# Kernel optimization log

Hardware: AMD Instinct MI355X
Metric: run time of the kernel (lower is better)

Reference implementation:

```python
import jax, jax.numpy as jnp
import numpy as np


def setup_inputs() -> dict:
    key = jax.random.key(0)
    B, L, H, D = 4, 4096, 8, 64
    sample_k = int(np.ceil(np.log(L)))  # factor=1 -> U_part = ceil(ln L_K) = 9
    k1, k2, k3, k4 = jax.random.split(key, 4)
    return {
        "queries": jax.random.normal(k1, (B, L, H, D), jnp.float32),
        "keys": jax.random.normal(k2, (B, L, H, D), jnp.float32),
        "values": jax.random.normal(k3, (B, L, H, D), jnp.float32),
        "index_sample": jax.random.randint(k4, (L, sample_k), 0, L),
    }


def _prob_attention(Q, K, V, index_sample):
    # Q, K, V: [B, H, L, D]
    B, H, L_K, D = K.shape
    L_Q = Q.shape[2]
    u = min(int(np.ceil(np.log(L_Q))), L_Q)  # n_top (static)

    # --- _prob_QK: sampled scores, sparsity measure M, top-u queries ---
    # gather sampled keys per query position: [B, H, L_Q, sample_k, D]
    K_sample = K[:, :, index_sample, :]
    QK_sample = jnp.einsum('bhld,bhlsd->bhls', Q, K_sample)  # [B,H,L_Q,S]
    M = QK_sample.max(axis=-1) - QK_sample.sum(axis=-1) / L_K  # [B,H,L_Q]
    _, M_top = jax.lax.top_k(M, u)  # [B,H,u] indices of top queries

    Q_reduce = jnp.take_along_axis(Q, M_top[..., None], axis=2)  # [B,H,u,D]
    scale = 1.0 / jnp.sqrt(jnp.asarray(D, Q.dtype))
    scores = jnp.einsum('bhud,bhkd->bhuk', Q_reduce, K) * scale  # [B,H,u,L_K]

    # --- initial context (mask_flag=False): mean of V over keys ---
    context = jnp.broadcast_to(V.mean(axis=2, keepdims=True), (B, H, L_Q, D))

    # --- update context at the top-u query positions ---
    attn = jax.nn.softmax(scores, axis=-1)  # [B,H,u,L_K]
    ctx_top = jnp.einsum('bhuk,bhkd->bhud', attn, V)  # [B,H,u,D]
    b_idx = jnp.arange(B)[:, None, None]
    h_idx = jnp.arange(H)[None, :, None]
    context = context.at[b_idx, h_idx, M_top].set(ctx_top)
    return context, attn


def reference(queries, keys, values, index_sample):
    # inputs: [B, L, H, D] -> internal [B, H, L, D]
    Q = queries.transpose(0, 2, 1, 3)
    K = keys.transpose(0, 2, 1, 3)
    V = values.transpose(0, 2, 1, 3)
    context, attn = _prob_attention(Q, K, V, index_sample)
    return context.transpose(0, 2, 1, 3), attn
```

## Files before the change

kernel.cpp:

```cpp
#include <hip/hip_runtime.h>
#include <math.h>

#define B_ 4
#define L_ 4096
#define H_ 8
#define D_ 64
#define S_ 9
#define U_ 9
#define VC_ 64
#define CC_ 16
#define TKC_ 8
#define KCH_ 32
#define SCB_ (B_ * (L_ / KCH_))

#define VMBLK_ 256
#define MBLK_ 4096
#define FILLBLK_ 8192

__device__ __forceinline__ float dot4(const float4& a, const float4& b) {
    return a.x * b.x + a.y * b.y + a.z * b.z + a.w * b.w;
}

__global__ void __launch_bounds__(256, 4)
kernel_M_vmean(const float* __restrict__ Q, const float* __restrict__ K,
               const int* __restrict__ idx, float* __restrict__ M,
               const float* __restrict__ V, float* __restrict__ vpart) {
    if (blockIdx.x < VMBLK_) {
        int blk = blockIdx.x;
        int c = blk & (VC_ - 1), b = blk >> 6;
        int col = threadIdx.x & 127;
        int lp  = threadIdx.x >> 7;
        const int CHUNK = L_ / VC_;
        const float4* base = (const float4*)(V + (size_t)b * L_ * H_ * D_);
        float4 acc = make_float4(0.f, 0.f, 0.f, 0.f);
        for (int l = c * CHUNK + lp; l < (c + 1) * CHUNK; l += 2) {
            float4 v = base[(size_t)l * 128 + col];
            acc.x += v.x; acc.y += v.y; acc.z += v.z; acc.w += v.w;
        }
        __shared__ float4 red[256];
        red[threadIdx.x] = acc;
        __syncthreads();
        if (lp == 0) {
            float4 o = red[threadIdx.x + 128];
            acc.x += o.x; acc.y += o.y; acc.z += o.z; acc.w += o.w;
            ((float4*)vpart)[(size_t)blk * 128 + col] = acc;
        }
        return;
    }
    int t = threadIdx.x;
    int wid = t >> 6, lane = t & 63;
    int w = ((blockIdx.x - VMBLK_) << 2) + wid;
    int b = __builtin_amdgcn_readfirstlane(w >> 12);
    int l = __builtin_amdgcn_readfirstlane(w & (L_ - 1));

    int ki[S_];
#pragma unroll
    for (int s = 0; s < S_; ++s) ki[s] = idx[l * S_ + s];

    const float4* qb = (const float4*)(Q + (size_t)(b * L_ + l) * (H_ * D_));
    float4 q0 = qb[2 * lane];
    float4 q1 = qb[2 * lane + 1];

    const float* Kb = K + (size_t)b * L_ * (H_ * D_);

    float4 ka[S_], kc[S_];
#pragma unroll
    for (int s = 0; s < S_; ++s) {
        const float4* kp = (const float4*)(Kb + (size_t)ki[s] * (H_ * D_));
        ka[s] = kp[2 * lane];
        kc[s] = kp[2 * lane + 1];
    }

    float mx = -INFINITY, sm = 0.0f;
#pragma unroll
    for (int s = 0; s < S_; ++s) {
        float d = dot4(q0, ka[s]) + dot4(q1, kc[s]);
        d += __shfl_xor(d, 1);
        d += __shfl_xor(d, 2);
        d += __shfl_xor(d, 4);
        mx = fmaxf(mx, d);
        sm += d;
    }
    if ((lane & 7) == 0) {
        int h = lane >> 3;
        M[((size_t)(b * H_ + h) << 12) + l] = mx - sm * (1.0f / (float)L_);
    }
}

#define CSWAP(a, b)                                                          \
    if (v[b] > v[a] || (v[b] == v[a] && id[b] < id[a])) {                    \
        float tv = v[a]; v[a] = v[b]; v[b] = tv;                             \
        int ti = id[a]; id[a] = id[b]; id[b] = ti;                           \
    }

__global__ void kernel_topk1(const float* __restrict__ M,
                             float* __restrict__ cand_v, int* __restrict__ cand_i) {
    int bh = blockIdx.x >> 3;
    int chunk = blockIdx.x & (TKC_ - 1);
    int lane = threadIdx.x;
    const float* Ms = M + ((size_t)bh << 12);

    float v[8]; int id[8];
#pragma unroll
    for (int c = 0; c < 8; ++c) {
        int gi = chunk * 512 + lane + 64 * c;
        v[c] = Ms[gi]; id[c] = gi;
    }
    CSWAP(0,1) CSWAP(2,3) CSWAP(4,5) CSWAP(6,7)
    CSWAP(0,2) CSWAP(1,3) CSWAP(4,6) CSWAP(5,7)
    CSWAP(1,2) CSWAP(5,6)
    CSWAP(0,4) CSWAP(1,5) CSWAP(2,6) CSWAP(3,7)
    CSWAP(2,4) CSWAP(3,5)
    CSWAP(1,2) CSWAP(3,4) CSWAP(5,6)

    float* cv = cand_v + (size_t)blockIdx.x * U_;
    int*   ci = cand_i + (size_t)blockIdx.x * U_;
#pragma unroll
    for (int r = 0; r < U_; ++r) {
        float bv = v[0]; int bi = id[0];
#pragma unroll
        for (int off = 1; off < 64; off <<= 1) {
            float ov = __shfl_xor(bv, off);
            int   oi = __shfl_xor(bi, off);
            if (ov > bv || (ov == bv && oi < bi)) { bv = ov; bi = oi; }
        }
        if (lane == 0) { cv[r] = bv; ci[r] = bi; }
        if (id[0] == bi) {
#pragma unroll
            for (int c = 0; c < 7; ++c) { v[c] = v[c+1]; id[c] = id[c+1]; }
            v[7] = -INFINITY; id[7] = 0x7fffffff;
        }
    }
}

__global__ void kernel_small(const float* __restrict__ cand_v, const int* __restrict__ cand_i,
                             int* __restrict__ Mtop, const float* __restrict__ vpart,
                             float* __restrict__ vmean) {
    if (blockIdx.x >= 32) {
        int bh = blockIdx.x - 32;
        int h = bh & (H_ - 1), b = bh >> 3;
        int d = threadIdx.x;
        float s = 0.0f;
        for (int c = 0; c < VC_; ++c)
            s += vpart[(size_t)(b * VC_ + c) * (H_ * D_) + h * D_ + d];
        vmean[bh * D_ + d] = s * (1.0f / (float)L_);
        return;
    }
    int bh = blockIdx.x;
    int lane = threadIdx.x;
    const float* cv = cand_v + (size_t)bh * (TKC_ * U_);
    const int*   ci = cand_i + (size_t)bh * (TKC_ * U_);

    float v[2]; int id[2];
    v[0] = cv[lane]; id[0] = ci[lane];
    if (lane < TKC_ * U_ - 64) { v[1] = cv[64 + lane]; id[1] = ci[64 + lane]; }
    else { v[1] = -INFINITY; id[1] = 0x7fffffff; }
    CSWAP(0,1)

#pragma unroll
    for (int r = 0; r < U_; ++r) {
        float bv = v[0]; int bi = id[0];
#pragma unroll
        for (int off = 1; off < 64; off <<= 1) {
            float ov = __shfl_xor(bv, off);
            int   oi = __shfl_xor(bi, off);
            if (ov > bv || (ov == bv && oi < bi)) { bv = ov; bi = oi; }
        }
        if (lane == 0) Mtop[bh * U_ + r] = bi;
        if (id[0] == bi) { v[0] = v[1]; id[0] = id[1]; v[1] = -INFINITY; id[1] = 0x7fffffff; }
    }
}

__global__ void __launch_bounds__(256, 4)
kernel_fill_scores(float* __restrict__ out, const float* __restrict__ vmean,
                   const float* __restrict__ Q, const float* __restrict__ K,
                   const int* __restrict__ Mtop, float* __restrict__ raw) {
    if (blockIdx.x < FILLBLK_) {
        int i = blockIdx.x * 256 + threadIdx.x;
        int d4 = i & 15;
        int h  = (i >> 4) & (H_ - 1);
        int b  = i >> (4 + 3 + 12);
        ((float4*)out)[i] = ((const float4*)vmean)[(b * H_ + h) * 16 + d4];
        return;
    }
    int n = blockIdx.x - FILLBLK_;
    int b = n >> 7;
    int chunk = n & 127;
    int k0 = chunk * KCH_;

    int t = threadIdx.x;
    int w = t >> 6, lane = t & 63;
    int h = lane >> 3, dq = lane & 7;
    int bh = b * H_ + h;

    float4 q0[U_], q1[U_];
#pragma unroll
    for (int u = 0; u < U_; ++u) {
        int mi = Mtop[bh * U_ + u];
        const float4* qp = (const float4*)(Q + (size_t)((b * L_ + mi) * H_ + h) * D_);
        q0[u] = qp[2 * dq];
        q1[u] = qp[2 * dq + 1];
    }

    __shared__ float sc[H_][U_][KCH_ + 1];

    const float* Kb = K + (size_t)b * L_ * (H_ * D_);
    const float4* kp = (const float4*)(Kb + (size_t)(k0 + w * 8) * (H_ * D_));
    float4 kv0 = kp[2 * lane], kv1 = kp[2 * lane + 1];
#pragma unroll
    for (int i = 0; i < 8; ++i) {
        int kloc = w * 8 + i;
        float4 nv0, nv1;
        if (i < 7) {
            const float4* np = (const float4*)(Kb + (size_t)(k0 + kloc + 1) * (H_ * D_));
            nv0 = np[2 * lane]; nv1 = np[2 * lane + 1];
        }
        float p[U_];
#pragma unroll
        for (int u = 0; u < U_; ++u) {
            float d = dot4(q0[u], kv0) + dot4(q1[u], kv1);
            d += __shfl_xor(d, 1);
            d += __shfl_xor(d, 2);
            d += __shfl_xor(d, 4);
            p[u] = d;
        }
        float val = p[0];
#pragma unroll
        for (int u = 1; u < 8; ++u) val = (dq == u) ? p[u] : val;
        sc[h][dq][kloc] = val;
        if (dq == 0) sc[h][8][kloc] = p[8];
        kv0 = nv0; kv1 = nv1;
    }
    __syncthreads();

#pragma unroll
    for (int r = 0; r < 9; ++r) {
        int j = r * 256 + t;
        int kloc = j & 31;
        int hu = j >> 5;
        int h2 = hu / U_, u2 = hu - h2 * U_;
        raw[((size_t)(b * H_ + h2) * U_ + u2) * L_ + k0 + kloc] =
            sc[h2][u2][kloc] * 0.125f;
    }
}

__global__ void kernel_softmax(float* __restrict__ attn) {
    int row = blockIdx.x;
    float4* a = (float4*)(attn + (size_t)row * L_);
    int t = threadIdx.x;

    float4 v[4];
    float mx = -INFINITY;
#pragma unroll
    for (int i = 0; i < 4; ++i) {
        v[i] = a[t + 256 * i];
        mx = fmaxf(mx, fmaxf(fmaxf(v[i].x, v[i].y), fmaxf(v[i].z, v[i].w)));
    }
    __shared__ float red[256];
    __shared__ float bmax, bsum;
    red[t] = mx;
    __syncthreads();
    for (int off = 128; off > 0; off >>= 1) {
        if (t < off) red[t] = fmaxf(red[t], red[t + off]);
        __syncthreads();
    }
    if (t == 0) bmax = red[0];
    __syncthreads();

    float mm = bmax, sum = 0.0f;
#pragma unroll
    for (int i = 0; i < 4; ++i) {
        v[i].x = expf(v[i].x - mm); v[i].y = expf(v[i].y - mm);
        v[i].z = expf(v[i].z - mm); v[i].w = expf(v[i].w - mm);
        sum += v[i].x + v[i].y + v[i].z + v[i].w;
    }
    red[t] = sum;
    __syncthreads();
    for (int off = 128; off > 0; off >>= 1) {
        if (t < off) red[t] += red[t + off];
        __syncthreads();
    }
    if (t == 0) bsum = red[0];
    __syncthreads();

    float inv = 1.0f / bsum;
#pragma unroll
    for (int i = 0; i < 4; ++i) {
        v[i].x *= inv; v[i].y *= inv; v[i].z *= inv; v[i].w *= inv;
        a[t + 256 * i] = v[i];
    }
}

__global__ void kernel_ctxf(const float* __restrict__ attn, const float* __restrict__ V,
                            float* __restrict__ cpart) {
    int n = blockIdx.x;
    int x = n & 7, m = n >> 3;
    int chunk = m & (CC_ - 1);
    int bh = (m >> 4) * 8 + x;
    int h = bh & (H_ - 1), b = bh >> 3;
    int k0 = chunk * (L_ / CC_);

    int t = threadIdx.x;
    int g = t >> 6, lane = t & 63;
    int kl = lane >> 4, d4 = lane & 15;
    const float* abase = attn + (size_t)bh * U_ * L_;

    float4 acc[U_];
#pragma unroll
    for (int u = 0; u < U_; ++u) acc[u] = make_float4(0.f, 0.f, 0.f, 0.f);

    for (int i = 0; i < 16; ++i) {
        int k = k0 + (g * 4 + kl) + 16 * i;
        float4 vv = *(const float4*)(V + (size_t)((b * L_ + k) * H_ + h) * D_ + 4 * d4);
        float av[U_];
#pragma unroll
        for (int u = 0; u < U_; ++u) av[u] = abase[(size_t)u * L_ + k];
#pragma unroll
        for (int u = 0; u < U_; ++u) {
            acc[u].x += av[u] * vv.x; acc[u].y += av[u] * vv.y;
            acc[u].z += av[u] * vv.z; acc[u].w += av[u] * vv.w;
        }
    }
#pragma unroll
    for (int u = 0; u < U_; ++u) {
        acc[u].x += __shfl_xor(acc[u].x, 16); acc[u].y += __shfl_xor(acc[u].y, 16);
        acc[u].z += __shfl_xor(acc[u].z, 16); acc[u].w += __shfl_xor(acc[u].w, 16);
        acc[u].x += __shfl_xor(acc[u].x, 32); acc[u].y += __shfl_xor(acc[u].y, 32);
        acc[u].z += __shfl_xor(acc[u].z, 32); acc[u].w += __shfl_xor(acc[u].w, 32);
    }
    __shared__ float4 red[U_][4][16];
    if (kl == 0) {
#pragma unroll
        for (int u = 0; u < U_; ++u) red[u][g][d4] = acc[u];
    }
    __syncthreads();
    if (t < U_ * 16) {
        int u = t >> 4, dd = t & 15;
        float4 s0 = red[u][0][dd], s1 = red[u][1][dd];
        float4 s2 = red[u][2][dd], s3 = red[u][3][dd];
        float4 s = make_float4(s0.x + s1.x + s2.x + s3.x, s0.y + s1.y + s2.y + s3.y,
                               s0.z + s1.z + s2.z + s3.z, s0.w + s1.w + s2.w + s3.w);
        ((float4*)cpart)[((size_t)(bh * CC_ + chunk) * U_ + u) * 16 + dd] = s;
    }
}

__global__ void kernel_ctx2(const float* __restrict__ cpart, const int* __restrict__ Mtop,
                            float* __restrict__ out) {
    int row = blockIdx.x;
    int u = row % U_, bh = row / U_;
    int h = bh & (H_ - 1), b = bh >> 3;
    int d = threadIdx.x;
    float s = 0.0f;
#pragma unroll
    for (int c = 0; c < CC_; ++c)
        s += cpart[((size_t)(bh * CC_ + c) * U_ + u) * 64 + d];
    int l = Mtop[bh * U_ + u];
    out[(size_t)((b * L_ + l) * H_ + h) * D_ + d] = s;
}

extern "C" void kernel_launch(void* const* d_in, const int* in_sizes, int n_in,
                              void* d_out, int out_size, void* d_ws, size_t ws_size,
                              hipStream_t stream) {
    const float* Q   = (const float*)d_in[0];
    const float* K   = (const float*)d_in[1];
    const float* V   = (const float*)d_in[2];
    const int*   idx = (const int*)d_in[3];

    float* ctx_out  = (float*)d_out;
    float* attn_out = (float*)d_out + (size_t)B_ * L_ * H_ * D_;

    float* M      = (float*)d_ws;
    float* vpart  = M + (size_t)B_ * H_ * L_;
    float* vmean  = vpart + (size_t)B_ * VC_ * H_ * D_;
    float* cpart  = vmean + B_ * H_ * D_;
    float* cand_v = cpart + (size_t)32 * CC_ * U_ * 64;
    int*   cand_i = (int*)(cand_v + 32 * TKC_ * U_);
    int*   Mtop   = cand_i + 32 * TKC_ * U_;

    kernel_M_vmean<<<VMBLK_ + MBLK_, 256, 0, stream>>>(Q, K, idx, M, V, vpart);
    kernel_topk1<<<B_ * H_ * TKC_, 64, 0, stream>>>(M, cand_v, cand_i);
    kernel_small<<<64, 64, 0, stream>>>(cand_v, cand_i, Mtop, vpart, vmean);
    kernel_fill_scores<<<FILLBLK_ + SCB_, 256, 0, stream>>>(ctx_out, vmean, Q, K, Mtop, attn_out);
    kernel_softmax<<<B_ * H_ * U_, 256, 0, stream>>>(attn_out);
    kernel_ctxf<<<32 * CC_, 256, 0, stream>>>(attn_out, V, cpart);
    kernel_ctx2<<<B_ * H_ * U_, 64, 0, stream>>>(cpart, Mtop, ctx_out);
}
```

Before: 195.7 us.

## Fuse softmax into score and context kernels using per-chunk online max/sum stats

Removes the standalone softmax kernel. The score kernel now writes per-chunk (max, sum-exp) statistics for each 32-key chunk. The context kernel merges these into global softmax stats, normalizes its slice of attention in place, and stages it in shared memory for the V product. This drops one launch and one full read/write pass over attention, at the cost of redundant stat merging in every ctx block and extra expf work.

```diff
diff --git a/kernel.cpp b/kernel.cpp
--- a/kernel.cpp
+++ b/kernel.cpp
@@ -11,7 +11,8 @@
 #define CC_ 16
 #define TKC_ 8
 #define KCH_ 32
-#define SCB_ (B_ * (L_ / KCH_))
+#define NCHK_ (L_ / KCH_)
+#define SCB_ (B_ * NCHK_)
 
 #define VMBLK_ 256
 #define MBLK_ 4096
@@ -174,7 +175,8 @@
 __global__ void __launch_bounds__(256, 4)
 kernel_fill_scores(float* __restrict__ out, const float* __restrict__ vmean,
                    const float* __restrict__ Q, const float* __restrict__ K,
-                   const int* __restrict__ Mtop, float* __restrict__ raw) {
+                   const int* __restrict__ Mtop, float* __restrict__ raw,
+                   float* __restrict__ stats) {
     if (blockIdx.x < FILLBLK_) {
         int i = blockIdx.x * 256 + threadIdx.x;
         int d4 = i & 15;
@@ -242,57 +244,23 @@
         raw[((size_t)(b * H_ + h2) * U_ + u2) * L_ + k0 + kloc] =
             sc[h2][u2][kloc] * 0.125f;
     }
-}
-
-__global__ void kernel_softmax(float* __restrict__ attn) {
-    int row = blockIdx.x;
-    float4* a = (float4*)(attn + (size_t)row * L_);
-    int t = threadIdx.x;
-
-    float4 v[4];
-    float mx = -INFINITY;
-#pragma unroll
-    for (int i = 0; i < 4; ++i) {
-        v[i] = a[t + 256 * i];
-        mx = fmaxf(mx, fmaxf(fmaxf(v[i].x, v[i].y), fmaxf(v[i].z, v[i].w)));
-    }
-    __shared__ float red[256];
-    __shared__ float bmax, bsum;
-    red[t] = mx;
-    __syncthreads();
-    for (int off = 128; off > 0; off >>= 1) {
-        if (t < off) red[t] = fmaxf(red[t], red[t + off]);
-        __syncthreads();
-    }
-    if (t == 0) bmax = red[0];
-    __syncthreads();
-
-    float mm = bmax, sum = 0.0f;
-#pragma unroll
-    for (int i = 0; i < 4; ++i) {
-        v[i].x = expf(v[i].x - mm); v[i].y = expf(v[i].y - mm);
-        v[i].z = expf(v[i].z - mm); v[i].w = expf(v[i].w - mm);
-        sum += v[i].x + v[i].y + v[i].z + v[i].w;
-    }
-    red[t] = sum;
-    __syncthreads();
-    for (int off = 128; off > 0; off >>= 1) {
-        if (t < off) red[t] += red[t + off];
-        __syncthreads();
-    }
-    if (t == 0) bsum = red[0];
-    __syncthreads();
-
-    float inv = 1.0f / bsum;
-#pragma unroll
-    for (int i = 0; i < 4; ++i) {
-        v[i].x *= inv; v[i].y *= inv; v[i].z *= inv; v[i].w *= inv;
-        a[t + 256 * i] = v[i];
-    }
-}
-
-__global__ void kernel_ctxf(const float* __restrict__ attn, const float* __restrict__ V,
-                            float* __restrict__ cpart) {
+
+    if (t < H_ * U_) {
+        int h2 = t / U_, u2 = t - h2 * U_;
+        float mxs = -INFINITY;
+#pragma unroll
+        for (int k = 0; k < KCH_; ++k) mxs = fmaxf(mxs, sc[h2][u2][k]);
+        mxs *= 0.125f;
+        float se = 0.0f;
+#pragma unroll
+        for (int k = 0; k < KCH_; ++k) se += expf(sc[h2][u2][k] * 0.125f - mxs);
+        ((float2*)stats)[(size_t)((b * H_ + h2) * U_ + u2) * NCHK_ + chunk] =
+            make_float2(mxs, se);
+    }
+}
+
+__global__ void kernel_ctxf(float* __restrict__ attn, const float* __restrict__ stats,
+                            const float* __restrict__ V, float* __restrict__ cpart) {
     int n = blockIdx.x;
     int x = n & 7, m = n >> 3;
     int chunk = m & (CC_ - 1);
@@ -301,20 +269,57 @@
     int k0 = chunk * (L_ / CC_);
 
     int t = threadIdx.x;
+
+    __shared__ float2 gstat[U_];
+    int j = t & 31;
+    for (int u = t >> 5; u < U_; u += 8) {
+        const float2* srow = (const float2*)stats + (size_t)(bh * U_ + u) * NCHK_;
+        float2 a = srow[j];
+        float mm = a.x, ss = a.y;
+#pragma unroll
+        for (int c = 1; c < 4; ++c) {
+            float2 b2 = srow[j + 32 * c];
+            float nm = fmaxf(mm, b2.x);
+            ss = ss * expf(mm - nm) + b2.y * expf(b2.x - nm);
+            mm = nm;
+        }
+#pragma unroll
+        for (int off = 1; off < 32; off <<= 1) {
+            float om = __shfl_xor(mm, off, 32);
+            float os = __shfl_xor(ss, off, 32);
+            float nm = fmaxf(mm, om);
+            ss = ss * expf(mm - nm) + os * expf(om - nm);
+            mm = nm;
+        }
+        if (j == 0) gstat[u] = make_float2(mm, 1.0f / ss);
+    }
+    __syncthreads();
+
+    __shared__ float attn_s[U_][256];
+    float* arow = attn + (size_t)bh * U_ * L_ + k0;
+#pragma unroll
+    for (int u = 0; u < U_; ++u) {
+        float xv = arow[(size_t)u * L_ + t];
+        float av = expf(xv - gstat[u].x) * gstat[u].y;
+        attn_s[u][t] = av;
+        arow[(size_t)u * L_ + t] = av;
+    }
+    __syncthreads();
+
     int g = t >> 6, lane = t & 63;
     int kl = lane >> 4, d4 = lane & 15;
-    const float* abase = attn + (size_t)bh * U_ * L_;
 
     float4 acc[U_];
 #pragma unroll
     for (int u = 0; u < U_; ++u) acc[u] = make_float4(0.f, 0.f, 0.f, 0.f);
 
     for (int i = 0; i < 16; ++i) {
-        int k = k0 + (g * 4 + kl) + 16 * i;
+        int kloc = (g * 4 + kl) + 16 * i;
+        int k = k0 + kloc;
         float4 vv = *(const float4*)(V + (size_t)((b * L_ + k) * H_ + h) * D_ + 4 * d4);
         float av[U_];
 #pragma unroll
-        for (int u = 0; u < U_; ++u) av[u] = abase[(size_t)u * L_ + k];
+        for (int u = 0; u < U_; ++u) av[u] = attn_s[u][kloc];
 #pragma unroll
         for (int u = 0; u < U_; ++u) {
             acc[u].x += av[u] * vv.x; acc[u].y += av[u] * vv.y;
@@ -376,12 +381,13 @@
     float* cand_v = cpart + (size_t)32 * CC_ * U_ * 64;
     int*   cand_i = (int*)(cand_v + 32 * TKC_ * U_);
     int*   Mtop   = cand_i + 32 * TKC_ * U_;
+    float* stats  = (float*)(Mtop + 32 * U_);
 
     kernel_M_vmean<<<VMBLK_ + MBLK_, 256, 0, stream>>>(Q, K, idx, M, V, vpart);
     kernel_topk1<<<B_ * H_ * TKC_, 64, 0, stream>>>(M, cand_v, cand_i);
     kernel_small<<<64, 64, 0, stream>>>(cand_v, cand_i, Mtop, vpart, vmean);
-    kernel_fill_scores<<<FILLBLK_ + SCB_, 256, 0, stream>>>(ctx_out, vmean, Q, K, Mtop, attn_out);
-    kernel_softmax<<<B_ * H_ * U_, 256, 0, stream>>>(attn_out);
-    kernel_ctxf<<<32 * CC_, 256, 0, stream>>>(attn_out, V, cpart);
+    kernel_fill_scores<<<FILLBLK_ + SCB_, 256, 0, stream>>>(ctx_out, vmean, Q, K, Mtop,
+                                                            attn_out, stats);
+    kernel_ctxf<<<32 * CC_, 256, 0, stream>>>(attn_out, stats, V, cpart);
     kernel_ctx2<<<B_ * H_ * U_, 64, 0, stream>>>(cpart, Mtop, ctx_out);
 }
```

Measured after the change: 193.3 us, median of 3. About the same (-1.2%).
